# Performance work log

Measured on AMD Instinct MI355X. Metric: run time of the kernel, lower is better.

## Reference

```python
import jax, jax.numpy as jnp
import numpy as np

N_SENT = 100000   # source ('sent') nodes
N_TYPE = 10000    # destination ('type') nodes
E = 640000        # edges of etype 'has'
D = 128           # out_dim
LEAKY_SLOPE = 0.01  # F.leaky_relu default


def setup_inputs() -> dict:
    key = jax.random.key(0)
    k0, k1, k2, k3, k4 = jax.random.split(key, 5)
    h_sent = jax.random.normal(k0, (N_SENT, D), jnp.float32)
    h_type = jax.random.normal(k1, (N_TYPE, D), jnp.float32)
    # attn_fc: Linear(2*D, 1, bias=False) -> weight [1, 2*D]
    attn_w = jax.random.normal(k2, (1, 2 * D), jnp.float32) * (1.0 / np.sqrt(2 * D))
    src_idx = jax.random.randint(k3, (E,), 0, N_SENT, dtype=jnp.int32)
    dst_idx = jax.random.randint(k4, (E,), 0, N_TYPE, dtype=jnp.int32)
    return {"h_sent": h_sent, "h_type": h_type, "attn_w": attn_w,
            "src_idx": src_idx, "dst_idx": dst_idx}


def reference(h_sent, h_type, attn_w, src_idx, dst_idx):
    w = attn_w[0]  # [2D]
    # attn_fc(cat(src_h, dst_h)) == src_h @ w[:D] + dst_h @ w[D:]  (no bias)
    s_src = h_sent @ w[:D]   # [N_SENT]
    s_dst = h_type @ w[D:]   # [N_TYPE]
    e = jax.nn.leaky_relu(s_src[src_idx] + s_dst[dst_idx], LEAKY_SLOPE)  # [E]
    # segment (per-destination) softmax over incoming edges
    m = jax.ops.segment_max(e, dst_idx, num_segments=N_TYPE)             # [N_TYPE]
    m = jnp.where(jnp.isfinite(m), m, 0.0)                               # empty segments -> 0
    ex = jnp.exp(e - m[dst_idx])                                         # [E]
    denom = jax.ops.segment_sum(ex, dst_idx, num_segments=N_TYPE)        # [N_TYPE]
    alpha = ex / denom[dst_idx]                                          # [E]
    # weighted scatter-sum of source features into destination nodes
    msg = alpha[:, None] * h_sent[src_idx]                               # [E, D]
    h_new = jax.ops.segment_sum(msg, dst_idx, num_segments=N_TYPE)       # [N_TYPE, D]
    # DGL only updates nodes that received messages; isolated nodes keep h
    deg = jax.ops.segment_sum(jnp.ones_like(e), dst_idx, num_segments=N_TYPE)
    return jnp.where(deg[:, None] > 0, h_new, h_type)
```

## Files before the change

### kernel.cpp

```cpp
#include <hip/hip_runtime.h>
#include <stdint.h>
#include <stddef.h>

#define N_SENT 100000
#define N_TYPE 10000
#define NEDGE  640000
#define NROWS  (N_SENT + N_TYPE)
#define MAXDEG 256
#define HB     256
#define HCHUNK (NEDGE / HB)

__device__ __forceinline__ float bf2f(uint32_t lo16) {
    return __builtin_bit_cast(float, lo16 << 16);
}
__device__ __forceinline__ uint32_t f2bf(float f) {
    uint32_t u = __builtin_bit_cast(uint32_t, f);
    return (u + 0x7fffu + ((u >> 16) & 1u)) >> 16;
}

__device__ __forceinline__ bool detect_bf16(const uint32_t* __restrict__ h) {
    uint32_t u = h[threadIdx.x & 63];
    uint32_t e_lo = (u >> 7) & 0xffu;
    int ok = (e_lo >= 100u && e_lo <= 140u) ? 1 : 0;
    unsigned long long m = __ballot(ok);
    return __popcll(m) >= 48;
}

#define SCORE_BLOCKS ((NROWS + 63) / 64)

__global__ __launch_bounds__(256) void scores_k(const void* __restrict__ h_sent,
                                                const void* __restrict__ h_type,
                                                const void* __restrict__ attn_w,
                                                float* __restrict__ s_src,
                                                float* __restrict__ s_dst) {
    int lane = threadIdx.x & 63;
    int r0   = (blockIdx.x * 4 + (int)(threadIdx.x >> 6)) * 16;
    bool isbf = detect_bf16((const uint32_t*)h_sent);
    float v[16];
    if (isbf) {
        uint32_t wv_s = ((const uint32_t*)attn_w)[lane];
        uint32_t wv_t = ((const uint32_t*)attn_w)[64 + lane];
        float ws0 = bf2f(wv_s & 0xffffu), ws1 = bf2f(wv_s >> 16);
        float wt0 = bf2f(wv_t & 0xffffu), wt1 = bf2f(wv_t >> 16);
        uint32_t hv[16];
#pragma unroll
        for (int i = 0; i < 16; i++) {
            int g  = r0 + i;
            int gc = g < NROWS ? g : NROWS - 1;
            bool isSrc = gc < N_SENT;
            const uint32_t* hp = isSrc
                ? (const uint32_t*)h_sent + (size_t)gc * 64
                : (const uint32_t*)h_type + (size_t)(gc - N_SENT) * 64;
            hv[i] = hp[lane];
        }
        __builtin_amdgcn_sched_barrier(0);
#pragma unroll
        for (int i = 0; i < 16; i++) {
            int g = r0 + i;
            bool isSrc = g < N_SENT;
            float wa = isSrc ? ws0 : wt0, wb = isSrc ? ws1 : wt1;
            v[i] = (g < NROWS)
                 ? (bf2f(hv[i] & 0xffffu) * wa + bf2f(hv[i] >> 16) * wb)
                 : 0.0f;
        }
    } else {
        float2 wv_s = ((const float2*)attn_w)[lane];
        float2 wv_t = ((const float2*)attn_w)[64 + lane];
        float2 hv[16];
#pragma unroll
        for (int i = 0; i < 16; i++) {
            int g  = r0 + i;
            int gc = g < NROWS ? g : NROWS - 1;
            bool isSrc = gc < N_SENT;
            const float2* hp = isSrc
                ? (const float2*)h_sent + (size_t)gc * 64
                : (const float2*)h_type + (size_t)(gc - N_SENT) * 64;
            hv[i] = hp[lane];
        }
        __builtin_amdgcn_sched_barrier(0);
#pragma unroll
        for (int i = 0; i < 16; i++) {
            int g = r0 + i;
            bool isSrc = g < N_SENT;
            float wa = isSrc ? wv_s.x : wv_t.x, wb = isSrc ? wv_s.y : wv_t.y;
            v[i] = (g < NROWS) ? (hv[i].x * wa + hv[i].y * wb) : 0.0f;
        }
    }
    int b0 = lane & 1, b1 = (lane >> 1) & 1, b2 = (lane >> 2) & 1, b3 = (lane >> 3) & 1;
    float w_[8];
#pragma unroll
    for (int i = 0; i < 8; i++) {
        float keep = b0 ? v[2 * i + 1] : v[2 * i];
        float send = b0 ? v[2 * i]     : v[2 * i + 1];
        w_[i] = keep + __shfl_xor(send, 1, 64);
    }
    float x_[4];
#pragma unroll
    for (int i = 0; i < 4; i++) {
        float keep = b1 ? w_[2 * i + 1] : w_[2 * i];
        float send = b1 ? w_[2 * i]     : w_[2 * i + 1];
        x_[i] = keep + __shfl_xor(send, 2, 64);
    }
    float y_[2];
#pragma unroll
    for (int i = 0; i < 2; i++) {
        float keep = b2 ? x_[2 * i + 1] : x_[2 * i];
        float send = b2 ? x_[2 * i]     : x_[2 * i + 1];
        y_[i] = keep + __shfl_xor(send, 4, 64);
    }
    float z;
    {
        float keep = b3 ? y_[1] : y_[0];
        float send = b3 ? y_[0] : y_[1];
        z = keep + __shfl_xor(send, 8, 64);
    }
    z += __shfl_xor(z, 16, 64);
    z += __shfl_xor(z, 32, 64);
    if (lane < 16) {
        int g = r0 + lane;
        if (g < NROWS) {
            if (g < N_SENT) s_src[g] = z;
            else            s_dst[g - N_SENT] = z;
        }
    }
}

__global__ __launch_bounds__(256) void count_k(const int* __restrict__ dst,
                                               uint32_t* __restrict__ count2) {
    __shared__ uint32_t hist[N_TYPE];
    int cb = blockIdx.x;
    int t  = threadIdx.x;
#pragma unroll
    for (int i = 0; i < 40; i++) {
        int idx = i * 256 + t;
        if (idx < N_TYPE) hist[idx] = 0u;
    }
    __syncthreads();
    int e0 = cb * HCHUNK;
    int dv[10];
#pragma unroll
    for (int k = 0; k < 10; k++) {
        int i = k * 256 + t;
        dv[k] = dst[e0 + (i < HCHUNK ? i : HCHUNK - 1)];
    }
    __builtin_amdgcn_sched_barrier(0);
#pragma unroll
    for (int k = 0; k < 10; k++) {
        int i = k * 256 + t;
        if (i < HCHUNK) atomicAdd(&hist[dv[k]], 1u);
    }
    __syncthreads();
    uint4* row = (uint4*)(count2 + (size_t)cb * N_TYPE);
#pragma unroll
    for (int i = 0; i < 10; i++) {
        int idx = i * 256 + t;
        if (idx < N_TYPE / 4) row[idx] = ((const uint4*)hist)[idx];
    }
}

__global__ __launch_bounds__(256) void sumscan_k(uint32_t* __restrict__ count2,
                                                 uint32_t* __restrict__ total) {
    int b = blockIdx.x * 256 + (int)threadIdx.x;
    bool ok = b < N_TYPE;
    int bc = ok ? b : N_TYPE - 1;
    uint32_t run = 0;
#pragma unroll
    for (int g = 0; g < HB / 64; g++) {
        uint32_t vals[64];
#pragma unroll
        for (int c = 0; c < 64; c++)
            vals[c] = count2[(size_t)(g * 64 + c) * N_TYPE + bc];
        __builtin_amdgcn_sched_barrier(0);
#pragma unroll
        for (int c = 0; c < 64; c++) { uint32_t v = vals[c]; vals[c] = run; run += v; }
        if (ok) {
#pragma unroll
            for (int c = 0; c < 64; c++)
                count2[(size_t)(g * 64 + c) * N_TYPE + b] = vals[c];
        }
    }
    if (ok) total[b] = run;
}

__global__ __launch_bounds__(1024) void scan_k(const uint32_t* __restrict__ total,
                                               uint32_t* __restrict__ offsets) {
    const int CH = 10;
    int t = threadIdx.x, lane = t & 63, wv = t >> 6;
    int base = t * CH;
    uint32_t local[CH];
    uint32_t tsum = 0;
#pragma unroll
    for (int i = 0; i < CH; i++) {
        int idx = base + i;
        uint32_t c = (idx < N_TYPE) ? total[idx] : 0u;
        local[i] = c;
        tsum += c;
    }
    uint32_t orig = tsum;
#pragma unroll
    for (int off = 1; off < 64; off <<= 1) {
        uint32_t v = __shfl_up(tsum, off, 64);
        if (lane >= off) tsum += v;
    }
    __shared__ uint32_t wsum[16];
    if (lane == 63) wsum[wv] = tsum;
    __syncthreads();
    if (wv == 0 && lane < 16) {
        uint32_t u = wsum[lane], o = u;
#pragma unroll
        for (int off = 1; off < 16; off <<= 1) {
            uint32_t v = __shfl_up(u, off, 64);
            if (lane >= off) u += v;
        }
        wsum[lane] = u - o;
    }
    __syncthreads();
    uint32_t run = wsum[wv] + tsum - orig;
#pragma unroll
    for (int i = 0; i < CH; i++) {
        int idx = base + i;
        if (idx < N_TYPE) {
            offsets[idx] = run;
            run += local[i];
        } else if (idx == N_TYPE) {
            offsets[idx] = run;
        }
    }
}

__global__ __launch_bounds__(256) void fill_k(const int* __restrict__ src,
                                              const int* __restrict__ dst,
                                              const uint32_t* __restrict__ offsets,
                                              const uint32_t* __restrict__ base2,
                                              uint32_t* __restrict__ edge_src) {
    __shared__ uint32_t cur[N_TYPE];
    int cb = blockIdx.x;
    int t  = threadIdx.x;
    const uint32_t* brow = base2 + (size_t)cb * N_TYPE;
#pragma unroll
    for (int i = 0; i < 10; i++) {
        int idx = i * 256 + t;
        if (idx < N_TYPE / 4) {
            uint4 o = ((const uint4*)offsets)[idx];
            uint4 b = ((const uint4*)brow)[idx];
            uint4 c; c.x = o.x + b.x; c.y = o.y + b.y; c.z = o.z + b.z; c.w = o.w + b.w;
            ((uint4*)cur)[idx] = c;
        }
    }
    __syncthreads();
    int e0 = cb * HCHUNK;
    int dv[10], sv[10];
#pragma unroll
    for (int k = 0; k < 10; k++) {
        int i = k * 256 + t;
        int e = e0 + (i < HCHUNK ? i : HCHUNK - 1);
        dv[k] = dst[e];
        sv[k] = src[e];
    }
    __builtin_amdgcn_sched_barrier(0);
#pragma unroll
    for (int k = 0; k < 10; k++) {
        int i = k * 256 + t;
        if (i < HCHUNK) {
            uint32_t pos = atomicAdd(&cur[dv[k]], 1u);
            edge_src[pos] = (uint32_t)sv[k];
        }
    }
}

__global__ __launch_bounds__(256) void agg_k(const void* __restrict__ h_sent,
                                             const void* __restrict__ h_type,
                                             const float* __restrict__ s_src,
                                             const float* __restrict__ s_dst,
                                             const uint32_t* __restrict__ offsets,
                                             const uint32_t* __restrict__ edge_src,
                                             void* __restrict__ out) {
    __shared__ float    sc[4][MAXDEG];
    __shared__ uint32_t ss[4][MAXDEG];
    int j     = (blockIdx.x * 256 + threadIdx.x) >> 6;
    int wslot = threadIdx.x >> 6;
    int lane  = threadIdx.x & 63;
    bool valid = j < N_TYPE;
    bool isbf  = detect_bf16((const uint32_t*)h_sent);
    uint32_t beg = 0, deg = 0;
    float sdj = 0.0f;
    if (valid) {
        beg = offsets[j];
        deg = offsets[j + 1] - beg;
        sdj = s_dst[j];
    }
    float*    mysc = sc[wslot];
    uint32_t* myss = ss[wslot];
    bool fits = (deg <= MAXDEG);
    float m = -INFINITY;
    for (uint32_t k = lane; k < deg; k += 64) {
        uint32_t s = edge_src[beg + k];
        float v = s_src[s] + sdj;
        v = v > 0.0f ? v : 0.01f * v;
        if (fits) { mysc[k] = v; myss[k] = s; }
        m = fmaxf(m, v);
    }
#pragma unroll
    for (int off = 32; off; off >>= 1) m = fmaxf(m, __shfl_xor(m, off, 64));
    __syncthreads();
    if (!valid) return;
    if (deg == 0) {
        if (isbf) ((uint32_t*)out)[(size_t)j * 64 + lane] =
                      ((const uint32_t*)h_type)[(size_t)j * 64 + lane];
        else      ((float2*)out)[(size_t)j * 64 + lane] =
                      ((const float2*)h_type)[(size_t)j * 64 + lane];
        return;
    }
    float denom = 0.0f, a0 = 0.0f, a1 = 0.0f;
    if (isbf) {
        const uint32_t* hp = (const uint32_t*)h_sent;
        uint32_t k = 0;
        if (fits) {
            for (; k + 8 <= deg; k += 8) {
                uint32_t sv[8]; float vv[8]; uint32_t gv[8];
#pragma unroll
                for (int i = 0; i < 8; i++) { sv[i] = myss[k + i]; vv[i] = mysc[k + i]; }
#pragma unroll
                for (int i = 0; i < 8; i++) gv[i] = hp[(size_t)sv[i] * 64 + lane];
#pragma unroll
                for (int i = 0; i < 8; i++) {
                    float w = __expf(vv[i] - m);
                    denom += w;
                    a0 += w * bf2f(gv[i] & 0xffffu);
                    a1 += w * bf2f(gv[i] >> 16);
                }
            }
            for (; k < deg; ++k) {
                float w = __expf(mysc[k] - m);
                uint32_t g = hp[(size_t)myss[k] * 64 + lane];
                denom += w;
                a0 += w * bf2f(g & 0xffffu);
                a1 += w * bf2f(g >> 16);
            }
        } else {
            for (k = 0; k < deg; ++k) {
                uint32_t s = edge_src[beg + k];
                float v = s_src[s] + sdj; v = v > 0.0f ? v : 0.01f * v;
                float w = __expf(v - m);
                uint32_t g = hp[(size_t)s * 64 + lane];
                denom += w;
                a0 += w * bf2f(g & 0xffffu);
                a1 += w * bf2f(g >> 16);
            }
        }
        float inv = 1.0f / denom;
        ((uint32_t*)out)[(size_t)j * 64 + lane] = f2bf(a0 * inv) | (f2bf(a1 * inv) << 16);
    } else {
        const float2* hp = (const float2*)h_sent;
        uint32_t k = 0;
        if (fits) {
            for (; k + 8 <= deg; k += 8) {
                uint32_t sv[8]; float vv[8]; float2 gv[8];
#pragma unroll
                for (int i = 0; i < 8; i++) { sv[i] = myss[k + i]; vv[i] = mysc[k + i]; }
#pragma unroll
                for (int i = 0; i < 8; i++) gv[i] = hp[(size_t)sv[i] * 64 + lane];
#pragma unroll
                for (int i = 0; i < 8; i++) {
                    float w = __expf(vv[i] - m);
                    denom += w;
                    a0 += w * gv[i].x;
                    a1 += w * gv[i].y;
                }
            }
            for (; k < deg; ++k) {
                float w = __expf(mysc[k] - m);
                float2 g = hp[(size_t)myss[k] * 64 + lane];
                denom += w;
                a0 += w * g.x;
                a1 += w * g.y;
            }
        } else {
            for (k = 0; k < deg; ++k) {
                uint32_t s = edge_src[beg + k];
                float v = s_src[s] + sdj; v = v > 0.0f ? v : 0.01f * v;
                float w = __expf(v - m);
                float2 g = hp[(size_t)s * 64 + lane];
                denom += w;
                a0 += w * g.x;
                a1 += w * g.y;
            }
        }
        float inv = 1.0f / denom;
        ((float2*)out)[(size_t)j * 64 + lane] = make_float2(a0 * inv, a1 * inv);
    }
}

static inline size_t align_up(size_t x) { return (x + 255) & ~(size_t)255; }

extern "C" void kernel_launch(void* const* d_in, const int* in_sizes, int n_in,
                              void* d_out, int out_size, void* d_ws, size_t ws_size,
                              hipStream_t stream) {
    const void* h_sent = d_in[0];
    const void* h_type = d_in[1];
    const void* attn_w = d_in[2];
    const int* src_idx = (const int*)d_in[3];
    const int* dst_idx = (const int*)d_in[4];

    char* w = (char*)d_ws;
    float*    s_src     = (float*)w;    w += align_up((size_t)N_SENT * 4);
    float*    s_dst     = (float*)w;    w += align_up((size_t)N_TYPE * 4);
    uint32_t* count2    = (uint32_t*)w; w += align_up((size_t)HB * N_TYPE * 4);
    uint32_t* total     = (uint32_t*)w; w += align_up((size_t)N_TYPE * 4);
    uint32_t* offsets   = (uint32_t*)w; w += align_up((size_t)(N_TYPE + 1) * 4);
    uint32_t* edge_src  = (uint32_t*)w; w += align_up((size_t)NEDGE * 4);

    scores_k<<<SCORE_BLOCKS, 256, 0, stream>>>(h_sent, h_type, attn_w, s_src, s_dst);
    count_k<<<HB, 256, 0, stream>>>(dst_idx, count2);
    sumscan_k<<<(N_TYPE + 255) / 256, 256, 0, stream>>>(count2, total);
    scan_k<<<1, 1024, 0, stream>>>(total, offsets);
    fill_k<<<HB, 256, 0, stream>>>(src_idx, dst_idx, offsets, count2, edge_src);
    agg_k<<<(N_TYPE + 3) / 4, 256, 0, stream>>>(h_sent, h_type, s_src, s_dst,
                                                offsets, edge_src, d_out);
}
```

Measured before the change: 175.0 us.

## Rewrite score kernel with 16-byte vector loads and unroll aggregation gathers by 16

The score kernel now has each thread load a 16-byte vector, so each row is covered by a group of lanes that reduce with xor shuffles. This replaces the older 16-rows-per-wave transposed reduction. In the fp32 path each thread handles two rows' chunks, split across halves of the grid. The aggregation kernel gains a 16-wide unrolled gather loop ahead of the 8-wide one, to keep more independent row loads in flight. This costs more registers per thread and may lower occupancy.

```diff
diff --git a/kernel.cpp b/kernel.cpp
--- a/kernel.cpp
+++ b/kernel.cpp
@@ -26,101 +26,66 @@
     return __popcll(m) >= 48;
 }
 
-#define SCORE_BLOCKS ((NROWS + 63) / 64)
+#define SC_BLOCKS 6875
 
 __global__ __launch_bounds__(256) void scores_k(const void* __restrict__ h_sent,
                                                 const void* __restrict__ h_type,
                                                 const void* __restrict__ attn_w,
                                                 float* __restrict__ s_src,
                                                 float* __restrict__ s_dst) {
+    int t    = blockIdx.x * 256 + (int)threadIdx.x;
     int lane = threadIdx.x & 63;
-    int r0   = (blockIdx.x * 4 + (int)(threadIdx.x >> 6)) * 16;
     bool isbf = detect_bf16((const uint32_t*)h_sent);
-    float v[16];
     if (isbf) {
-        uint32_t wv_s = ((const uint32_t*)attn_w)[lane];
-        uint32_t wv_t = ((const uint32_t*)attn_w)[64 + lane];
-        float ws0 = bf2f(wv_s & 0xffffu), ws1 = bf2f(wv_s >> 16);
-        float wt0 = bf2f(wv_t & 0xffffu), wt1 = bf2f(wv_t >> 16);
-        uint32_t hv[16];
-#pragma unroll
-        for (int i = 0; i < 16; i++) {
-            int g  = r0 + i;
-            int gc = g < NROWS ? g : NROWS - 1;
-            bool isSrc = gc < N_SENT;
-            const uint32_t* hp = isSrc
-                ? (const uint32_t*)h_sent + (size_t)gc * 64
-                : (const uint32_t*)h_type + (size_t)(gc - N_SENT) * 64;
-            hv[i] = hp[lane];
-        }
+        uint4 wsv = ((const uint4*)attn_w)[lane & 15];
+        uint4 wtv = ((const uint4*)attn_w)[16 + (lane & 15)];
+        bool isSrc = t < N_SENT * 16;
+        const uint4* p = isSrc ? (const uint4*)h_sent + t
+                               : (const uint4*)h_type + (t - N_SENT * 16);
+        uint4 h = *p;
+        uint4 wv = isSrc ? wsv : wtv;
+        float s = bf2f(h.x & 0xffffu) * bf2f(wv.x & 0xffffu)
+                + bf2f(h.x >> 16)     * bf2f(wv.x >> 16)
+                + bf2f(h.y & 0xffffu) * bf2f(wv.y & 0xffffu)
+                + bf2f(h.y >> 16)     * bf2f(wv.y >> 16)
+                + bf2f(h.z & 0xffffu) * bf2f(wv.z & 0xffffu)
+                + bf2f(h.z >> 16)     * bf2f(wv.z >> 16)
+                + bf2f(h.w & 0xffffu) * bf2f(wv.w & 0xffffu)
+                + bf2f(h.w >> 16)     * bf2f(wv.w >> 16);
+        s += __shfl_xor(s, 1, 64);
+        s += __shfl_xor(s, 2, 64);
+        s += __shfl_xor(s, 4, 64);
+        s += __shfl_xor(s, 8, 64);
+        if ((lane & 15) == 0) {
+            int row = t >> 4;
+            if (row < N_SENT) s_src[row] = s;
+            else              s_dst[row - N_SENT] = s;
+        }
+    } else {
+        float4 wsv = ((const float4*)attn_w)[lane & 31];
+        float4 wtv = ((const float4*)attn_w)[32 + (lane & 31)];
+        const int HALF = NROWS * 16;
+        int it0 = t, it1 = t + HALF;
+        bool s0 = it0 < N_SENT * 32, s1 = it1 < N_SENT * 32;
+        const float4* p0 = s0 ? (const float4*)h_sent + it0
+                              : (const float4*)h_type + (it0 - N_SENT * 32);
+        const float4* p1 = s1 ? (const float4*)h_sent + it1
+                              : (const float4*)h_type + (it1 - N_SENT * 32);
+        float4 h0 = *p0;
+        float4 h1 = *p1;
         __builtin_amdgcn_sched_barrier(0);
-#pragma unroll
-        for (int i = 0; i < 16; i++) {
-            int g = r0 + i;
-            bool isSrc = g < N_SENT;
-            float wa = isSrc ? ws0 : wt0, wb = isSrc ? ws1 : wt1;
-            v[i] = (g < NROWS)
-                 ? (bf2f(hv[i] & 0xffffu) * wa + bf2f(hv[i] >> 16) * wb)
-                 : 0.0f;
-        }
-    } else {
-        float2 wv_s = ((const float2*)attn_w)[lane];
-        float2 wv_t = ((const float2*)attn_w)[64 + lane];
-        float2 hv[16];
-#pragma unroll
-        for (int i = 0; i < 16; i++) {
-            int g  = r0 + i;
-            int gc = g < NROWS ? g : NROWS - 1;
-            bool isSrc = gc < N_SENT;
-            const float2* hp = isSrc
-                ? (const float2*)h_sent + (size_t)gc * 64
-                : (const float2*)h_type + (size_t)(gc - N_SENT) * 64;
-            hv[i] = hp[lane];
-        }
-        __builtin_amdgcn_sched_barrier(0);
-#pragma unroll
-        for (int i = 0; i < 16; i++) {
-            int g = r0 + i;
-            bool isSrc = g < N_SENT;
-            float wa = isSrc ? wv_s.x : wv_t.x, wb = isSrc ? wv_s.y : wv_t.y;
-            v[i] = (g < NROWS) ? (hv[i].x * wa + hv[i].y * wb) : 0.0f;
-        }
-    }
-    int b0 = lane & 1, b1 = (lane >> 1) & 1, b2 = (lane >> 2) & 1, b3 = (lane >> 3) & 1;
-    float w_[8];
-#pragma unroll
-    for (int i = 0; i < 8; i++) {
-        float keep = b0 ? v[2 * i + 1] : v[2 * i];
-        float send = b0 ? v[2 * i]     : v[2 * i + 1];
-        w_[i] = keep + __shfl_xor(send, 1, 64);
-    }
-    float x_[4];
-#pragma unroll
-    for (int i = 0; i < 4; i++) {
-        float keep = b1 ? w_[2 * i + 1] : w_[2 * i];
-        float send = b1 ? w_[2 * i]     : w_[2 * i + 1];
-        x_[i] = keep + __shfl_xor(send, 2, 64);
-    }
-    float y_[2];
-#pragma unroll
-    for (int i = 0; i < 2; i++) {
-        float keep = b2 ? x_[2 * i + 1] : x_[2 * i];
-        float send = b2 ? x_[2 * i]     : x_[2 * i + 1];
-        y_[i] = keep + __shfl_xor(send, 4, 64);
-    }
-    float z;
-    {
-        float keep = b3 ? y_[1] : y_[0];
-        float send = b3 ? y_[0] : y_[1];
-        z = keep + __shfl_xor(send, 8, 64);
-    }
-    z += __shfl_xor(z, 16, 64);
-    z += __shfl_xor(z, 32, 64);
-    if (lane < 16) {
-        int g = r0 + lane;
-        if (g < NROWS) {
-            if (g < N_SENT) s_src[g] = z;
-            else            s_dst[g - N_SENT] = z;
+        float4 w0 = s0 ? wsv : wtv, w1 = s1 ? wsv : wtv;
+        float a = h0.x * w0.x + h0.y * w0.y + h0.z * w0.z + h0.w * w0.w;
+        float b = h1.x * w1.x + h1.y * w1.y + h1.z * w1.z + h1.w * w1.w;
+        a += __shfl_xor(a, 1, 64);  b += __shfl_xor(b, 1, 64);
+        a += __shfl_xor(a, 2, 64);  b += __shfl_xor(b, 2, 64);
+        a += __shfl_xor(a, 4, 64);  b += __shfl_xor(b, 4, 64);
+        a += __shfl_xor(a, 8, 64);  b += __shfl_xor(b, 8, 64);
+        a += __shfl_xor(a, 16, 64); b += __shfl_xor(b, 16, 64);
+        if ((lane & 31) == 0) {
+            int r0 = it0 >> 5, r1 = it1 >> 5;
+            if (r0 < N_SENT) s_src[r0] = a; else s_dst[r0 - N_SENT] = a;
+            if (r1 < N_SENT) s_src[r1] = b; else s_dst[r1 - N_SENT] = b;
         }
     }
 }
@@ -316,6 +281,20 @@
         const uint32_t* hp = (const uint32_t*)h_sent;
         uint32_t k = 0;
         if (fits) {
+            for (; k + 16 <= deg; k += 16) {
+                uint32_t sv[16]; float vv[16]; uint32_t gv[16];
+#pragma unroll
+                for (int i = 0; i < 16; i++) { sv[i] = myss[k + i]; vv[i] = mysc[k + i]; }
+#pragma unroll
+                for (int i = 0; i < 16; i++) gv[i] = hp[(size_t)sv[i] * 64 + lane];
+#pragma unroll
+                for (int i = 0; i < 16; i++) {
+                    float w = __expf(vv[i] - m);
+                    denom += w;
+                    a0 += w * bf2f(gv[i] & 0xffffu);
+                    a1 += w * bf2f(gv[i] >> 16);
+                }
+            }
             for (; k + 8 <= deg; k += 8) {
                 uint32_t sv[8]; float vv[8]; uint32_t gv[8];
 #pragma unroll
@@ -354,6 +333,20 @@
         const float2* hp = (const float2*)h_sent;
         uint32_t k = 0;
         if (fits) {
+            for (; k + 16 <= deg; k += 16) {
+                uint32_t sv[16]; float vv[16]; float2 gv[16];
+#pragma unroll
+                for (int i = 0; i < 16; i++) { sv[i] = myss[k + i]; vv[i] = mysc[k + i]; }
+#pragma unroll
+                for (int i = 0; i < 16; i++) gv[i] = hp[(size_t)sv[i] * 64 + lane];
+#pragma unroll
+                for (int i = 0; i < 16; i++) {
+                    float w = __expf(vv[i] - m);
+                    denom += w;
+                    a0 += w * gv[i].x;
+                    a1 += w * gv[i].y;
+                }
+            }
             for (; k + 8 <= deg; k += 8) {
                 uint32_t sv[8]; float vv[8]; float2 gv[8];
 #pragma unroll
@@ -410,7 +403,7 @@
     uint32_t* offsets   = (uint32_t*)w; w += align_up((size_t)(N_TYPE + 1) * 4);
     uint32_t* edge_src  = (uint32_t*)w; w += align_up((size_t)NEDGE * 4);
 
-    scores_k<<<SCORE_BLOCKS, 256, 0, stream>>>(h_sent, h_type, attn_w, s_src, s_dst);
+    scores_k<<<SC_BLOCKS, 256, 0, stream>>>(h_sent, h_type, attn_w, s_src, s_dst);
     count_k<<<HB, 256, 0, stream>>>(dst_idx, count2);
     sumscan_k<<<(N_TYPE + 255) / 256, 256, 0, stream>>>(count2, total);
     scan_k<<<1, 1024, 0, stream>>>(total, offsets);
```

After: 174.7 us. No clear change (-0.2%).
